# Optimization experiments

Measured on AMD Instinct MI355X. Metric: run time of the kernel, lower is better.

Reference implementation:

```python
import jax, jax.numpy as jnp
import numpy as np

B, S, E = 4, 2048, 1024
HIDDEN = 1024
HEADS = 16


def setup_inputs() -> dict:
    key = jax.random.key(0)
    k0, k1, k2, k3, k4 = jax.random.split(key, 5)
    inputs = jax.random.normal(k0, (B, S, E), dtype=jnp.float32)
    W_qkv = jax.random.normal(k1, (E, 3 * HIDDEN), dtype=jnp.float32) * 0.02
    b_qkv = jnp.zeros((3 * HIDDEN,), dtype=jnp.float32)
    W_out = jax.random.normal(k2, (HIDDEN, HIDDEN), dtype=jnp.float32) * 0.02
    b_out = jnp.zeros((HIDDEN,), dtype=jnp.float32)
    return {"inputs": inputs, "W_qkv": W_qkv, "b_qkv": b_qkv, "W_out": W_out, "b_out": b_out}


def reference(inputs, W_qkv, b_qkv, W_out, b_out):
    Bv, Sv, Ev = inputs.shape
    x = inputs @ W_qkv + b_qkv                      # [B, S, 3*hidden]
    # Faithful to the original: reshape mixes seq and hidden exactly as the source does.
    x = x.reshape(Bv, HEADS, Sv, -1)                # [B, H, S, 3*hidden/H]
    q, k, v = jnp.split(x, 3, axis=-1)              # each [B, H, S, hidden/H]
    scale = (2 * HIDDEN) ** (-0.5)
    qk = jnp.einsum('bhse,bhte->bhst', q, k) * scale  # [B, H, S, S]
    mask = jnp.triu(jnp.full((Sv, Sv), -jnp.inf, dtype=qk.dtype), k=1)
    attn = jax.nn.softmax(qk + mask, axis=-1)
    sa = jnp.einsum('bhst,bhte->bhse', attn, v).reshape(Bv, Sv, -1)  # [B, S, hidden]
    return sa @ W_out + b_out
```

## Files before the change

kernel.cpp:

```cpp
#include <hip/hip_runtime.h>
#include <hip/hip_bf16.h>

using bf16 = __hip_bfloat16;

typedef __attribute__((ext_vector_type(8))) short short8;
typedef __attribute__((ext_vector_type(4))) float f32x4;


#define CEXP 0.03188127742677263f

__device__ __forceinline__ unsigned short f2bf(float v) {
  bf16 h = __float2bfloat16(v);
  return *(unsigned short*)&h;
}
__device__ __forceinline__ unsigned int pack2bf(float a, float b) {
  return (unsigned int)f2bf(a) | ((unsigned int)f2bf(b) << 16);
}

__device__ __forceinline__ void gload_lds16(const void* g, void* lds) {
  __builtin_amdgcn_global_load_lds(
      (const __attribute__((address_space(1))) unsigned int*)(g),
      (__attribute__((address_space(3))) unsigned int*)(lds), 16, 0, 0);
}

__global__ void detect_kernel(const unsigned int* __restrict__ x, int* __restrict__ flag) {
  unsigned int w = x[threadIdx.x];
  unsigned int e = (w >> 7) & 0xFF;
  bool inband = (e >= 96 && e <= 133);
  unsigned long long m = __ballot(inband);
  if (threadIdx.x == 0) flag[0] = (__popcll(m) >= 48) ? 0 : 1;
}

__global__ __launch_bounds__(256) void convert_kernel(
    const void* __restrict__ src, bf16* __restrict__ dst, int n8,
    const int* __restrict__ flag) {
  int i = blockIdx.x * 256 + threadIdx.x;
  if (i >= n8) return;
  uint4 outv;
  if (*flag) {
    const float4* s = (const float4*)src + (size_t)i * 2;
    float4 a = s[0], b = s[1];
    outv.x = pack2bf(a.x, a.y);
    outv.y = pack2bf(a.z, a.w);
    outv.z = pack2bf(b.x, b.y);
    outv.w = pack2bf(b.z, b.w);
  } else {
    outv = ((const uint4*)src)[i];
  }
  ((uint4*)dst)[i] = outv;
}

__global__ void convert_bias_qkv(const void* __restrict__ src, bf16* __restrict__ dst,
                                 const int* __restrict__ flag) {
  int i = blockIdx.x * 256 + threadIdx.x;
  if (i >= 3072) return;
  float v = (*flag) ? ((const float*)src)[i]
                    : __bfloat162float(((const bf16*)src)[i]);
  if ((i % 192) < 64) v *= CEXP;
  dst[i] = __float2bfloat16(v);
}

__global__ __launch_bounds__(256) void transpose_bf16(
    const void* __restrict__ src, bf16* __restrict__ dst, int R, int Cc,
    const int* __restrict__ flag, int qscale) {
  __shared__ float tile[32][33];
  const int c0 = blockIdx.x * 32, r0 = blockIdx.y * 32;
  const int tx = threadIdx.x & 31, ty = threadIdx.x >> 5;
  const bool f32 = (*flag != 0);
#pragma unroll
  for (int it = 0; it < 4; ++it) {
    int r = ty + it * 8;
    float v;
    if (f32) v = ((const float*)src)[(size_t)(r0 + r) * Cc + c0 + tx];
    else     v = __bfloat162float(((const bf16*)src)[(size_t)(r0 + r) * Cc + c0 + tx]);
    tile[r][tx] = v;
  }
  __syncthreads();
#pragma unroll
  for (int it = 0; it < 4; ++it) {
    int r = ty + it * 8;
    float vv = tile[tx][r];
    if (qscale && (((c0 + r) % 192) < 64)) vv *= CEXP;
    dst[(size_t)(c0 + r) * R + r0 + tx] = __float2bfloat16(vv);
  }
}

__global__ __launch_bounds__(256) void transpose_v(const bf16* __restrict__ qkv,
                                                   bf16* __restrict__ vtg)
{
  __shared__ short tile[64][72];
  const int bh = blockIdx.x;
  const int k0 = blockIdx.y * 64;
  const unsigned short* qk = (const unsigned short*)qkv + (size_t)bh * 393216;
  const int key = threadIdx.x & 63;
  const int dv = threadIdx.x >> 6;
  const int gk = k0 + key;
  const unsigned short* src =
      qk + (size_t)(gk >> 4) * 3072 + (gk & 15) * 192 + 128 + dv * 16;
  *(short8*)&tile[key][dv * 16] = *(const short8*)src;
  *(short8*)&tile[key][dv * 16 + 8] = *(const short8*)(src + 8);
  __syncthreads();
  const int d = threadIdx.x & 63;
  const int kv = threadIdx.x >> 6;
  unsigned short* dst =
      (unsigned short*)vtg + ((size_t)bh * 64 + d) * 2048 + k0 + kv * 16;
  short8 a, b;
#pragma unroll
  for (int j = 0; j < 8; ++j) {
    a[j] = tile[kv * 16 + j][d];
    b[j] = tile[kv * 16 + 8 + j][d];
  }
  *(short8*)dst = a;
  *(short8*)(dst + 8) = b;
}

__global__ __launch_bounds__(512) void gemm256(
    const bf16* __restrict__ A, const bf16* __restrict__ BT,
    const bf16* __restrict__ bias, void* __restrict__ C,
    int M, int N, int K, int store_mode, const int* __restrict__ flag)
{
  __shared__ alignas(16) short As2[2][16384];
  __shared__ alignas(16) short Bs2[2][16384];
  const bool store_f32 = store_mode && (*flag != 0);
  const int tid = threadIdx.x;
  const int lane = tid & 63;
  const int w = tid >> 6;
  const int l15 = lane & 15, l4 = lane >> 4;
  const int wm2 = w >> 2, wn4 = w & 3;

  const int nwg = gridDim.x * gridDim.y;
  const int orig = blockIdx.x + gridDim.x * blockIdx.y;
  const int qn = nwg >> 3;
  const int swz = (orig & 7) * qn + (orig >> 3);
  const int bx = swz % gridDim.x, by = swz / gridDim.x;
  const int m0 = by * 256, n0 = bx * 256;

  const int srow = tid >> 3;
  const int koff = ((tid & 7) ^ (srow & 7)) << 3;
  const bf16* pa = A + (size_t)(m0 + srow) * K + koff;
  const bf16* pb = BT + (size_t)(n0 + srow) * K + koff;
  const int dst0 = tid * 8;

  const int rsw = l15 & 7;

  f32x4 acc[8][4] = {};
  const int nt = K >> 6;

#pragma unroll
  for (int q = 0; q < 4; ++q) {
    gload_lds16(pa + (size_t)(q * 64) * K, &As2[0][q * 4096 + dst0]);
    gload_lds16(pb + (size_t)(q * 64) * K, &Bs2[0][q * 4096 + dst0]);
  }

  for (int t = 0; t < nt; ++t) {
    const int c = t & 1;
    if (t + 1 < nt) {
      const int nb = c ^ 1;
      const bf16* sa_ = pa + (size_t)(t + 1) * 64;
      const bf16* sb_ = pb + (size_t)(t + 1) * 64;
#pragma unroll
      for (int q = 0; q < 4; ++q) {
        gload_lds16(sa_ + (size_t)(q * 64) * K, &As2[nb][q * 4096 + dst0]);
        gload_lds16(sb_ + (size_t)(q * 64) * K, &Bs2[nb][q * 4096 + dst0]);
      }
      asm volatile("s_waitcnt vmcnt(8)" ::: "memory");
    } else {
      asm volatile("s_waitcnt vmcnt(0)" ::: "memory");
    }
    __builtin_amdgcn_s_barrier();
    asm volatile("" ::: "memory");

#pragma unroll
    for (int s = 0; s < 2; ++s) {
      const int cgs = (((s << 2) | l4) ^ rsw) * 8;
      short8 af[8], bfr[4];
#pragma unroll
      for (int i = 0; i < 8; ++i)
        af[i] = *(const short8*)&As2[c][(wm2 * 128 + i * 16 + l15) * 64 + cgs];
#pragma unroll
      for (int j = 0; j < 4; ++j)
        bfr[j] = *(const short8*)&Bs2[c][(wn4 * 64 + j * 16 + l15) * 64 + cgs];
      __builtin_amdgcn_s_setprio(1);
#pragma unroll
      for (int i = 0; i < 8; ++i)
#pragma unroll
        for (int j = 0; j < 4; ++j)
          acc[i][j] = __builtin_amdgcn_mfma_f32_16x16x32_bf16(af[i], bfr[j], acc[i][j], 0, 0, 0);
      __builtin_amdgcn_s_setprio(0);
    }
    asm volatile("" ::: "memory");
    __builtin_amdgcn_s_barrier();
    asm volatile("" ::: "memory");
  }

#pragma unroll
  for (int j = 0; j < 4; ++j) {
    const int n = n0 + wn4 * 64 + j * 16 + l15;
    const float bv = __bfloat162float(bias[n]);
#pragma unroll
    for (int i = 0; i < 8; ++i) {
#pragma unroll
      for (int r = 0; r < 4; ++r) {
        const int mrow = m0 + wm2 * 128 + i * 16 + l4 * 4 + r;
        const float v = acc[i][j][r] + bv;
        if (store_f32) ((float*)C)[(size_t)mrow * N + n] = v;
        else           ((bf16*)C)[(size_t)mrow * N + n] = __float2bfloat16(v);
      }
    }
  }
}

__global__ __launch_bounds__(512) void attn_mfma(const bf16* __restrict__ qkv,
                                                 const bf16* __restrict__ vtg,
                                                 bf16* __restrict__ sa)
{
  __shared__ alignas(16) short Ks[2][4096];
  __shared__ alignas(16) short Vs[2][4096];
  __shared__ alignas(16) short Ps[8][1152];
  const int tid = threadIdx.x;
  const int bh = blockIdx.x;
  const int pr = blockIdx.y;
  const size_t base = (size_t)bh * 393216;
  const int w = tid >> 6;
  const int g = w >> 2;
  const int wl = w & 3;
  const int lane = tid & 63;
  const int l15 = lane & 15, l4 = lane >> 4;
  const unsigned short* qk = (const unsigned short*)qkv;
  const unsigned short* vtb = (const unsigned short*)vtg + (size_t)bh * 131072;
  short* psw = &Ps[w][0];

  const int qc = g ? pr : (15 - pr);
  const int my_ktmax  = 2 * qc + 1;
  const int blk_ktmax = 2 * (15 - pr) + 1;

  const unsigned short* gsrc0 =
      g ? (vtb + (size_t)lane * 2048)
        : (qk + base + (size_t)(lane >> 4) * 3072 + (lane & 15) * 192 + 64);
  const size_t gstep = g ? 64 : 12288;

  short8 qf[2][2];
#pragma unroll
  for (int h = 0; h < 2; ++h) {
    const unsigned short* pq =
        qk + base + (size_t)(qc * 8 + 2 * wl + h) * 3072 + l15 * 192 + l4 * 8;
    qf[h][0] = *(const short8*)pq;
    qf[h][1] = *(const short8*)(pq + 32);
  }

  f32x4 o[2][4] = {};
  float ml[2] = {-__builtin_inff(), -__builtin_inff()};
  float ls[2] = {0.f, 0.f};
  int cur = 0;

  {
    short* dstbuf = g ? &Vs[0][0] : &Ks[0][0];
    gload_lds16(gsrc0 + wl * 8, dstbuf + wl * 512);
    gload_lds16(gsrc0 + (wl + 4) * 8, dstbuf + (wl + 4) * 512);
  }
  __syncthreads();

  for (int kt = 0; kt <= blk_ktmax; ++kt) {
    if (kt < blk_ktmax) {
      short* dstbuf = g ? &Vs[cur ^ 1][0] : &Ks[cur ^ 1][0];
      const unsigned short* s = gsrc0 + (size_t)(kt + 1) * gstep;
      gload_lds16(s + wl * 8, dstbuf + wl * 512);
      gload_lds16(s + (wl + 4) * 8, dstbuf + (wl + 4) * 512);
    }

    if (kt <= my_ktmax) {
      f32x4 sc[2][4];
#pragma unroll
      for (int t = 0; t < 4; ++t) {
        const short8 kf0 = *(const short8*)&Ks[cur][(l4) * 512 + (16 * t + l15) * 8];
        const short8 kf1 = *(const short8*)&Ks[cur][(4 + l4) * 512 + (16 * t + l15) * 8];
#pragma unroll
        for (int h = 0; h < 2; ++h) {
          f32x4 c = {};
          c = __builtin_amdgcn_mfma_f32_16x16x32_bf16(kf0, qf[h][0], c, 0, 0, 0);
          c = __builtin_amdgcn_mfma_f32_16x16x32_bf16(kf1, qf[h][1], c, 0, 0, 0);
          sc[h][t] = c;
        }
      }

      if (kt >= 2 * qc) {
        const int kb = 64 * (kt - 2 * qc);
#pragma unroll
        for (int h = 0; h < 2; ++h) {
          const int thr = 32 * wl + 16 * h + l15;
#pragma unroll
          for (int t = 0; t < 4; ++t)
#pragma unroll
            for (int r = 0; r < 4; ++r)
              if (kb + 16 * t + 4 * l4 + r > thr) sc[h][t][r] = -__builtin_inff();
        }
      }

      unsigned int pk2[2][4][2];
#pragma unroll
      for (int h = 0; h < 2; ++h) {
        float mx = -__builtin_inff();
#pragma unroll
        for (int t = 0; t < 4; ++t)
#pragma unroll
          for (int r = 0; r < 4; ++r) mx = fmaxf(mx, sc[h][t][r]);
        mx = fmaxf(mx, __shfl_xor(mx, 16, 64));
        mx = fmaxf(mx, __shfl_xor(mx, 32, 64));
        if (!__all(mx <= ml[h] + 8.f)) {
          const float m_new = fmaxf(ml[h], mx);
          const float alpha = __builtin_amdgcn_exp2f(ml[h] - m_new);
          ml[h] = m_new;
          ls[h] *= alpha;
#pragma unroll
          for (int jn = 0; jn < 4; ++jn)
#pragma unroll
            for (int r = 0; r < 4; ++r) o[h][jn][r] *= alpha;
        }
        const float m_new = ml[h];
        float s = 0.f;
#pragma unroll
        for (int t = 0; t < 4; ++t) {
          float p0 = __builtin_amdgcn_exp2f(sc[h][t][0] - m_new);
          float p1 = __builtin_amdgcn_exp2f(sc[h][t][1] - m_new);
          float p2 = __builtin_amdgcn_exp2f(sc[h][t][2] - m_new);
          float p3 = __builtin_amdgcn_exp2f(sc[h][t][3] - m_new);
          s += (p0 + p1) + (p2 + p3);
          pk2[h][t][0] = pack2bf(p0, p1);
          pk2[h][t][1] = pack2bf(p2, p3);
        }
        s += __shfl_xor(s, 16, 64);
        s += __shfl_xor(s, 32, 64);
        ls[h] += s;
      }

      short8 pf[2][2];
#pragma unroll
      for (int h = 0; h < 2; ++h) {
#pragma unroll
        for (int t = 0; t < 4; ++t) {
          uint2 wv; wv.x = pk2[h][t][0]; wv.y = pk2[h][t][1];
          *(uint2*)(psw + l15 * 72 + 16 * t + 4 * l4) = wv;
        }
        pf[h][0] = *(const short8*)(psw + l15 * 72 + 8 * l4);
        pf[h][1] = *(const short8*)(psw + l15 * 72 + 32 + 8 * l4);
      }

#pragma unroll
      for (int jn = 0; jn < 4; ++jn)
#pragma unroll
        for (int ks = 0; ks < 2; ++ks) {
          const short8 vf =
              *(const short8*)&Vs[cur][(4 * ks + l4) * 512 + (16 * jn + l15) * 8];
#pragma unroll
          for (int h = 0; h < 2; ++h)
            o[h][jn] = __builtin_amdgcn_mfma_f32_16x16x32_bf16(vf, pf[h][ks], o[h][jn], 0, 0, 0);
        }
    }

    __syncthreads();
    cur ^= 1;
  }

#pragma unroll
  for (int h = 0; h < 2; ++h) {
    const float inv = 1.0f / ls[h];
    unsigned short* so =
        (unsigned short*)sa + (size_t)(bh * 128 + qc * 8 + 2 * wl + h) * 1024;
#pragma unroll
    for (int jn = 0; jn < 4; ++jn) {
      uint2 wv;
      wv.x = pack2bf(o[h][jn][0] * inv, o[h][jn][1] * inv);
      wv.y = pack2bf(o[h][jn][2] * inv, o[h][jn][3] * inv);
      *(uint2*)(so + l15 * 64 + jn * 16 + l4 * 4) = wv;
    }
  }
}

extern "C" void kernel_launch(void* const* d_in, const int* in_sizes, int n_in,
                              void* d_out, int out_size, void* d_ws, size_t ws_size,
                              hipStream_t stream)
{
  const void* x_raw    = d_in[0];
  const void* Wqkv_raw = d_in[1];
  const void* bqkv_raw = d_in[2];
  const void* Wout_raw = d_in[3];
  const void* bout_raw = d_in[4];

  char* ws = (char*)d_ws;
  int*  flag   = (int*)ws;
  bf16* xb     = (bf16*)(ws + 256);
  bf16* wqkvT  = xb + (size_t)8192 * 1024;
  bf16* bqkvb  = wqkvT + (size_t)3072 * 1024;
  bf16* woutT  = bqkvb + 4096;
  bf16* boutb  = woutT + (size_t)1024 * 1024;
  bf16* qkv    = boutb + 4096;
  bf16* sa     = qkv + (size_t)8192 * 3072;
  bf16* vtg    = sa + (size_t)8192 * 1024;

  detect_kernel<<<1, 64, 0, stream>>>((const unsigned int*)x_raw, flag);

  convert_kernel<<<(8192 * 1024 / 8 + 255) / 256, 256, 0, stream>>>(x_raw, xb, 8192 * 1024 / 8, flag);
  convert_bias_qkv<<<12, 256, 0, stream>>>(bqkv_raw, bqkvb, flag);
  convert_kernel<<<1, 256, 0, stream>>>(bout_raw, boutb, 1024 / 8, flag);
  transpose_bf16<<<dim3(3072 / 32, 1024 / 32), 256, 0, stream>>>(Wqkv_raw, wqkvT, 1024, 3072, flag, 1);
  transpose_bf16<<<dim3(1024 / 32, 1024 / 32), 256, 0, stream>>>(Wout_raw, woutT, 1024, 1024, flag, 0);

  gemm256<<<dim3(3072 / 256, 8192 / 256), 512, 0, stream>>>(
      xb, wqkvT, bqkvb, qkv, 8192, 3072, 1024, 0, flag);
  transpose_v<<<dim3(64, 32), 256, 0, stream>>>(qkv, vtg);
  attn_mfma<<<dim3(64, 8), 512, 0, stream>>>(qkv, vtg, sa);
  gemm256<<<dim3(1024 / 256, 8192 / 256), 512, 0, stream>>>(
      sa, woutT, boutb, d_out, 8192, 1024, 1024, 1, flag);
}
```

Measured before the change: 296.4 us.

## Template GEMM row tile; use 128-row tiles for output projection and split compute phases

```diff
diff --git a/kernel.cpp b/kernel.cpp
--- a/kernel.cpp
+++ b/kernel.cpp
@@ -114,12 +114,13 @@
   *(short8*)(dst + 8) = b;
 }
 
+template<int RI>
 __global__ __launch_bounds__(512) void gemm256(
     const bf16* __restrict__ A, const bf16* __restrict__ BT,
     const bf16* __restrict__ bias, void* __restrict__ C,
     int M, int N, int K, int store_mode, const int* __restrict__ flag)
 {
-  __shared__ alignas(16) short As2[2][16384];
+  __shared__ alignas(16) short As2[2][RI * 2048];
   __shared__ alignas(16) short Bs2[2][16384];
   const bool store_f32 = store_mode && (*flag != 0);
   const int tid = threadIdx.x;
@@ -133,7 +134,7 @@
   const int qn = nwg >> 3;
   const int swz = (orig & 7) * qn + (orig >> 3);
   const int bx = swz % gridDim.x, by = swz / gridDim.x;
-  const int m0 = by * 256, n0 = bx * 256;
+  const int m0 = by * (RI * 32), n0 = bx * 256;
 
   const int srow = tid >> 3;
   const int koff = ((tid & 7) ^ (srow & 7)) << 3;
@@ -143,14 +144,15 @@
 
   const int rsw = l15 & 7;
 
-  f32x4 acc[8][4] = {};
+  f32x4 acc[RI][4] = {};
   const int nt = K >> 6;
 
 #pragma unroll
-  for (int q = 0; q < 4; ++q) {
+  for (int q = 0; q < RI / 2; ++q)
     gload_lds16(pa + (size_t)(q * 64) * K, &As2[0][q * 4096 + dst0]);
+#pragma unroll
+  for (int q = 0; q < 4; ++q)
     gload_lds16(pb + (size_t)(q * 64) * K, &Bs2[0][q * 4096 + dst0]);
-  }
 
   for (int t = 0; t < nt; ++t) {
     const int c = t & 1;
@@ -159,38 +161,49 @@
       const bf16* sa_ = pa + (size_t)(t + 1) * 64;
       const bf16* sb_ = pb + (size_t)(t + 1) * 64;
 #pragma unroll
-      for (int q = 0; q < 4; ++q) {
+      for (int q = 0; q < RI / 2; ++q)
         gload_lds16(sa_ + (size_t)(q * 64) * K, &As2[nb][q * 4096 + dst0]);
+#pragma unroll
+      for (int q = 0; q < 4; ++q)
         gload_lds16(sb_ + (size_t)(q * 64) * K, &Bs2[nb][q * 4096 + dst0]);
-      }
-      asm volatile("s_waitcnt vmcnt(8)" ::: "memory");
+      if constexpr (RI == 8)
+        asm volatile("s_waitcnt vmcnt(8)" ::: "memory");
+      else
+        asm volatile("s_waitcnt vmcnt(6)" ::: "memory");
     } else {
       asm volatile("s_waitcnt vmcnt(0)" ::: "memory");
     }
     __builtin_amdgcn_s_barrier();
     asm volatile("" ::: "memory");
 
-#pragma unroll
-    for (int s = 0; s < 2; ++s) {
+    short8 bfr[4];
+#pragma unroll
+    for (int ph = 0; ph < 4; ++ph) {
+      const int s = ph >> 1, qi = ph & 1;
       const int cgs = (((s << 2) | l4) ^ rsw) * 8;
-      short8 af[8], bfr[4];
-#pragma unroll
-      for (int i = 0; i < 8; ++i)
-        af[i] = *(const short8*)&As2[c][(wm2 * 128 + i * 16 + l15) * 64 + cgs];
-#pragma unroll
-      for (int j = 0; j < 4; ++j)
-        bfr[j] = *(const short8*)&Bs2[c][(wn4 * 64 + j * 16 + l15) * 64 + cgs];
+      if (qi == 0) {
+#pragma unroll
+        for (int j = 0; j < 4; ++j)
+          bfr[j] = *(const short8*)&Bs2[c][(wn4 * 64 + j * 16 + l15) * 64 + cgs];
+      }
+      short8 af[RI / 2];
+#pragma unroll
+      for (int i2 = 0; i2 < RI / 2; ++i2)
+        af[i2] = *(const short8*)
+            &As2[c][(wm2 * (RI * 16) + qi * (RI * 8) + i2 * 16 + l15) * 64 + cgs];
       __builtin_amdgcn_s_setprio(1);
 #pragma unroll
-      for (int i = 0; i < 8; ++i)
+      for (int i2 = 0; i2 < RI / 2; ++i2)
 #pragma unroll
         for (int j = 0; j < 4; ++j)
-          acc[i][j] = __builtin_amdgcn_mfma_f32_16x16x32_bf16(af[i], bfr[j], acc[i][j], 0, 0, 0);
+          acc[qi * (RI / 2) + i2][j] =
+              __builtin_amdgcn_mfma_f32_16x16x32_bf16(af[i2], bfr[j],
+                                                      acc[qi * (RI / 2) + i2][j], 0, 0, 0);
       __builtin_amdgcn_s_setprio(0);
-    }
-    asm volatile("" ::: "memory");
-    __builtin_amdgcn_s_barrier();
-    asm volatile("" ::: "memory");
+      asm volatile("" ::: "memory");
+      __builtin_amdgcn_s_barrier();
+      asm volatile("" ::: "memory");
+    }
   }
 
 #pragma unroll
@@ -198,10 +211,10 @@
     const int n = n0 + wn4 * 64 + j * 16 + l15;
     const float bv = __bfloat162float(bias[n]);
 #pragma unroll
-    for (int i = 0; i < 8; ++i) {
+    for (int i = 0; i < RI; ++i) {
 #pragma unroll
       for (int r = 0; r < 4; ++r) {
-        const int mrow = m0 + wm2 * 128 + i * 16 + l4 * 4 + r;
+        const int mrow = m0 + wm2 * (RI * 16) + i * 16 + l4 * 4 + r;
         const float v = acc[i][j][r] + bv;
         if (store_f32) ((float*)C)[(size_t)mrow * N + n] = v;
         else           ((bf16*)C)[(size_t)mrow * N + n] = __float2bfloat16(v);
@@ -405,10 +418,10 @@
   transpose_bf16<<<dim3(3072 / 32, 1024 / 32), 256, 0, stream>>>(Wqkv_raw, wqkvT, 1024, 3072, flag, 1);
   transpose_bf16<<<dim3(1024 / 32, 1024 / 32), 256, 0, stream>>>(Wout_raw, woutT, 1024, 1024, flag, 0);
 
-  gemm256<<<dim3(3072 / 256, 8192 / 256), 512, 0, stream>>>(
+  gemm256<8><<<dim3(3072 / 256, 8192 / 256), 512, 0, stream>>>(
       xb, wqkvT, bqkvb, qkv, 8192, 3072, 1024, 0, flag);
   transpose_v<<<dim3(64, 32), 256, 0, stream>>>(qkv, vtg);
   attn_mfma<<<dim3(64, 8), 512, 0, stream>>>(qkv, vtg, sa);
-  gemm256<<<dim3(1024 / 256, 8192 / 256), 512, 0, stream>>>(
+  gemm256<4><<<dim3(1024 / 256, 8192 / 128), 512, 0, stream>>>(
       sa, woutT, boutb, d_out, 8192, 1024, 1024, 1, flag);
 }
```

New measurement: 290.1 us. -2.1%, faster.
